# Kernel tuning notes

Measured on AMD Instinct MI355X. Metric: run time of the kernel, lower is better.

## Reference

```python
import jax, jax.numpy as jnp
import numpy as np

SHAPES = ((100, 100), (50, 50), (25, 25), (13, 13))
LENS = [h * w for h, w in SHAPES]
STARTS = [0]
for n in LENS[:-1]:
    STARTS.append(STARTS[-1] + n)
S_TOT = sum(LENS)  # 13294
B, C, HH, DH, L, P, NQ, NL, FF = 2, 256, 8, 32, 4, 4, 300, 6, 1024
WH = np.array([[w, h] for h, w in SHAPES], np.float32)  # [L,2] (W,H) offset normalizer


def ln(x, g, b):
    m = x.mean(-1, keepdims=True)
    v = ((x - m) ** 2).mean(-1, keepdims=True)
    return (x - m) * jax.lax.rsqrt(v + 1e-5) * g + b


def bilinear(v, grid):
    # v: [N,Hl,Wl,D]; grid: [N,Q,2] in [-1,1]; grid_sample bilinear, align_corners=False, zero padding
    N, Hl, Wl, Dd = v.shape
    x = (grid[..., 0] + 1.0) * 0.5 * Wl - 0.5
    y = (grid[..., 1] + 1.0) * 0.5 * Hl - 0.5
    x0f = jnp.floor(x); y0f = jnp.floor(y)
    wx = x - x0f; wy = y - y0f
    x0 = x0f.astype(jnp.int32); y0 = y0f.astype(jnp.int32)
    vf = v.reshape(N, Hl * Wl, Dd)
    def g(yi, xi):
        valid = (yi >= 0) & (yi < Hl) & (xi >= 0) & (xi < Wl)
        idx = jnp.clip(yi, 0, Hl - 1) * Wl + jnp.clip(xi, 0, Wl - 1)
        return jnp.take_along_axis(vf, idx[..., None], axis=1) * valid[..., None]
    return (((1 - wy) * (1 - wx))[..., None] * g(y0, x0)
            + ((1 - wy) * wx)[..., None] * g(y0, x0 + 1)
            + (wy * (1 - wx))[..., None] * g(y0 + 1, x0)
            + (wy * wx)[..., None] * g(y0 + 1, x0 + 1))


def msda(query, ref, src, so_w, so_b, aw_w, aw_b, vp_w, vp_b, op_w, op_b):
    # query:[B,Lq,C] ref:[B,Lq,L,2] src:[B,S,C]
    Bq, Lq, _ = query.shape
    value = (src @ vp_w.T + vp_b).reshape(Bq, S_TOT, HH, DH)
    offs = (query @ so_w.T + so_b).reshape(Bq, Lq, HH, L, P, 2)
    aw = jax.nn.softmax((query @ aw_w.T + aw_b).reshape(Bq, Lq, HH, L * P), -1)
    aw = aw.reshape(Bq, Lq, HH, L, P)
    loc = ref[:, :, None, :, None, :] + offs / jnp.asarray(WH)[None, None, None, :, None, :]
    grid = 2.0 * loc - 1.0  # [B,Lq,HH,L,P,2]
    out = jnp.zeros((Bq, HH, Lq, DH), query.dtype)
    for l, (Hl, Wl) in enumerate(SHAPES):
        st = STARTS[l]
        v_l = value[:, st:st + Hl * Wl].reshape(Bq, Hl, Wl, HH, DH).transpose(0, 3, 1, 2, 4).reshape(Bq * HH, Hl, Wl, DH)
        g_l = grid[:, :, :, l].transpose(0, 2, 1, 3, 4).reshape(Bq * HH, Lq * P, 2)
        s = bilinear(v_l, g_l).reshape(Bq, HH, Lq, P, DH)
        out = out + jnp.einsum('bqhp,bhqpd->bhqd', aw[:, :, :, l], s)
    out = out.transpose(0, 2, 1, 3).reshape(Bq, Lq, C)
    return out @ op_w.T + op_b


def enc_ref_points():
    refs = []
    for Hl, Wl in SHAPES:
        ry = (jnp.arange(Hl, dtype=jnp.float32) + 0.5) / Hl
        rx = (jnp.arange(Wl, dtype=jnp.float32) + 0.5) / Wl
        gy, gx = jnp.meshgrid(ry, rx, indexing='ij')
        refs.append(jnp.stack([gx.reshape(-1), gy.reshape(-1)], -1))
    r = jnp.concatenate(refs, 0)  # [S,2]; valid_ratios == 1 (no padding)
    return jnp.broadcast_to(r[None, :, None, :], (B, S_TOT, L, 2))


def _forward(src_flatten, pos_flatten, query_embed, level_embed, refp_w, refp_b,
             eso_w, eso_b, eaw_w, eaw_b, evp_w, evp_b, eop_w, eop_b,
             en1_g, en1_b, el1_w, el1_b, el2_w, el2_b, en2_g, en2_b,
             dso_w, dso_b, daw_w, daw_b, dvp_w, dvp_b, dop_w, dop_b,
             dsa_in_w, dsa_in_b, dsa_out_w, dsa_out_b,
             dn1_g, dn1_b, dn2_g, dn2_b, dn3_g, dn3_b,
             dl1_w, dl1_b, dl2_w, dl2_b):
    lev = jnp.concatenate([jnp.broadcast_to(level_embed[l], (LENS[l], C)) for l in range(L)], 0)
    pos = pos_flatten + lev[None]
    memory = src_flatten
    eref = enc_ref_points()
    for i in range(NL):  # encoder
        q = memory + pos
        m2 = msda(q, eref, memory, eso_w[i], eso_b[i], eaw_w[i], eaw_b[i], evp_w[i], evp_b[i], eop_w[i], eop_b[i])
        memory = ln(memory + m2, en1_g[i], en1_b[i])
        f = jax.nn.relu(memory @ el1_w[i].T + el1_b[i]) @ el2_w[i].T + el2_b[i]
        memory = ln(memory + f, en2_g[i], en2_b[i])
    qpos, tgt = jnp.split(query_embed, 2, axis=-1)
    qpos = jnp.broadcast_to(qpos[None], (B, NQ, C))
    tgt = jnp.broadcast_to(tgt[None], (B, NQ, C))
    ref = jax.nn.sigmoid(qpos @ refp_w.T + refp_b)  # [B,NQ,2]
    init_ref = ref
    ref_in = jnp.broadcast_to(ref[:, :, None, :], (B, NQ, L, 2))
    scale = 1.0 / np.sqrt(DH)
    for i in range(NL):  # decoder
        q = tgt + qpos
        wq, wk, wv = jnp.split(dsa_in_w[i], 3, 0)
        bq, bk, bv = jnp.split(dsa_in_b[i], 3, 0)
        qh = (q @ wq.T + bq).reshape(B, NQ, HH, DH).transpose(0, 2, 1, 3)
        kh = (q @ wk.T + bk).reshape(B, NQ, HH, DH).transpose(0, 2, 1, 3)
        vh = (tgt @ wv.T + bv).reshape(B, NQ, HH, DH).transpose(0, 2, 1, 3)
        att = jax.nn.softmax(jnp.einsum('bhqd,bhkd->bhqk', qh, kh) * scale, -1)
        sa = jnp.einsum('bhqk,bhkd->bhqd', att, vh).transpose(0, 2, 1, 3).reshape(B, NQ, C)
        sa = sa @ dsa_out_w[i].T + dsa_out_b[i]
        tgt = ln(tgt + sa, dn2_g[i], dn2_b[i])
        ca = msda(tgt + qpos, ref_in, memory, dso_w[i], dso_b[i], daw_w[i], daw_b[i], dvp_w[i], dvp_b[i], dop_w[i], dop_b[i])
        tgt = ln(tgt + ca, dn1_g[i], dn1_b[i])
        f = jax.nn.relu(tgt @ dl1_w[i].T + dl1_b[i]) @ dl2_w[i].T + dl2_b[i]
        tgt = ln(tgt + f, dn3_g[i], dn3_b[i])
    return tgt, init_ref, ref


def setup_inputs() -> dict:
    ks = iter(jax.random.split(jax.random.key(0), 80))
    def rn(shape, s=0.02):
        return jax.random.normal(next(ks), shape, jnp.float32) * s
    z = lambda shape: jnp.zeros(shape, jnp.float32)
    o = lambda shape: jnp.ones(shape, jnp.float32)
    HLP2, HLP = HH * L * P * 2, HH * L * P
    return {
        'src_flatten': rn((B, S_TOT, C), 1.0),
        'pos_flatten': rn((B, S_TOT, C), 1.0),
        'query_embed': rn((NQ, 2 * C), 1.0),
        'level_embed': rn((L, C), 1.0),
        'refp_w': rn((2, C)), 'refp_b': z((2,)),
        'eso_w': rn((NL, HLP2, C)), 'eso_b': z((NL, HLP2)),
        'eaw_w': rn((NL, HLP, C)), 'eaw_b': z((NL, HLP)),
        'evp_w': rn((NL, C, C)), 'evp_b': z((NL, C)),
        'eop_w': rn((NL, C, C)), 'eop_b': z((NL, C)),
        'en1_g': o((NL, C)), 'en1_b': z((NL, C)),
        'el1_w': rn((NL, FF, C)), 'el1_b': z((NL, FF)),
        'el2_w': rn((NL, C, FF)), 'el2_b': z((NL, C)),
        'en2_g': o((NL, C)), 'en2_b': z((NL, C)),
        'dso_w': rn((NL, HLP2, C)), 'dso_b': z((NL, HLP2)),
        'daw_w': rn((NL, HLP, C)), 'daw_b': z((NL, HLP)),
        'dvp_w': rn((NL, C, C)), 'dvp_b': z((NL, C)),
        'dop_w': rn((NL, C, C)), 'dop_b': z((NL, C)),
        'dsa_in_w': rn((NL, 3 * C, C)), 'dsa_in_b': z((NL, 3 * C)),
        'dsa_out_w': rn((NL, C, C)), 'dsa_out_b': z((NL, C)),
        'dn1_g': o((NL, C)), 'dn1_b': z((NL, C)),
        'dn2_g': o((NL, C)), 'dn2_b': z((NL, C)),
        'dn3_g': o((NL, C)), 'dn3_b': z((NL, C)),
        'dl1_w': rn((NL, FF, C)), 'dl1_b': z((NL, FF)),
        'dl2_w': rn((NL, C, FF)), 'dl2_b': z((NL, C)),
    }


def reference(src_flatten, pos_flatten, query_embed, level_embed, refp_w, refp_b,
              eso_w, eso_b, eaw_w, eaw_b, evp_w, evp_b, eop_w, eop_b,
              en1_g, en1_b, el1_w, el1_b, el2_w, el2_b, en2_g, en2_b,
              dso_w, dso_b, daw_w, daw_b, dvp_w, dvp_b, dop_w, dop_b,
              dsa_in_w, dsa_in_b, dsa_out_w, dsa_out_b,
              dn1_g, dn1_b, dn2_g, dn2_b, dn3_g, dn3_b,
              dl1_w, dl1_b, dl2_w, dl2_b):
    return _forward(src_flatten, pos_flatten, query_embed, level_embed, refp_w, refp_b,
                    eso_w, eso_b, eaw_w, eaw_b, evp_w, evp_b, eop_w, eop_b,
                    en1_g, en1_b, el1_w, el1_b, el2_w, el2_b, en2_g, en2_b,
                    dso_w, dso_b, daw_w, daw_b, dvp_w, dvp_b, dop_w, dop_b,
                    dsa_in_w, dsa_in_b, dsa_out_w, dsa_out_b,
                    dn1_g, dn1_b, dn2_g, dn2_b, dn3_g, dn3_b,
                    dl1_w, dl1_b, dl2_w, dl2_b)
```

## Files before the change

kernel.cpp:

```cpp
#include <hip/hip_runtime.h>

static constexpr int kS  = 13294;
static constexpr int kB  = 2;
static constexpr int kBS = kB * kS;
static constexpr int kC  = 256;
static constexpr int kH  = 8;
static constexpr int kNQ = 300;
static constexpr int kFF = 1024;
static constexpr int kNL = 6;

using short8 = __attribute__((ext_vector_type(8))) short;
using f32x4  = __attribute__((ext_vector_type(4))) float;

__device__ __forceinline__ unsigned short f2b(float f) {
  unsigned u = __builtin_bit_cast(unsigned, f);
  return (unsigned short)((u + 0x7FFF + ((u >> 16) & 1)) >> 16);
}
__device__ __forceinline__ float bf2f(unsigned short u) {
  return __builtin_bit_cast(float, ((unsigned)u) << 16);
}
__device__ __forceinline__ float bflo(unsigned u) {
  return __builtin_bit_cast(float, u << 16);
}
__device__ __forceinline__ float bfhi(unsigned u) {
  return __builtin_bit_cast(float, u & 0xFFFF0000u);
}

#if defined(__has_builtin)
#if __has_builtin(__builtin_amdgcn_global_load_lds)
#define HAS_GLL 1
#endif
#endif
#ifndef HAS_GLL
#define HAS_GLL 0
#endif

#if HAS_GLL
typedef const __attribute__((address_space(1))) void* gas_t;
typedef __attribute__((address_space(3))) void* las_t;
#define GLOAD16(gp, lp) __builtin_amdgcn_global_load_lds((gas_t)(gp), (las_t)(lp), 16, 0, 0)
#endif


template<int ACT, int OBF>
__global__ __launch_bounds__(256) void gemm_mfma(
    const unsigned short* __restrict__ A, const unsigned short* __restrict__ Wt,
    const float* __restrict__ bias, void* __restrict__ outp, int M, int N, int K) {
  __shared__ __align__(16) unsigned short As[128 * 64];
  __shared__ __align__(16) unsigned short Bs[128 * 64];
  const int t = threadIdx.x;
  const int nB = N >> 7;
  const int tot = gridDim.x;
  const int q8 = tot >> 3, r8 = tot & 7;
  const int xcd = blockIdx.x & 7, pos = blockIdx.x >> 3;
  const int wg = (xcd < r8 ? xcd * (q8 + 1) : r8 * (q8 + 1) + (xcd - r8) * q8) + pos;
  const int m0 = (wg / nB) * 128, n0 = (wg % nB) * 128;
  const int wid = t >> 6, lane = t & 63;
  const int wr = wid >> 1, wc = wid & 1;
  const int srow = t >> 3;
  const int scol = (((t & 7) ^ (srow & 7)) * 8);
  const int lr = lane & 15;
  const int q4 = lane >> 4;
  const int e7 = lr & 7;

  f32x4 acc[4][4];
#pragma unroll
  for (int i = 0; i < 4; ++i)
#pragma unroll
    for (int j = 0; j < 4; ++j) acc[i][j] = (f32x4){0.f, 0.f, 0.f, 0.f};

  for (int k0 = 0; k0 < K; k0 += 64) {
#if HAS_GLL
    __syncthreads();
#pragma unroll
    for (int c = 0; c < 4; ++c) {
      int ar = m0 + c * 32 + srow; if (ar >= M) ar = M - 1;
      GLOAD16(A + (size_t)ar * K + k0 + scol, (char*)As + c * 4096 + t * 16);
      int br = n0 + c * 32 + srow; if (br >= N) br = N - 1;
      GLOAD16(Wt + (size_t)br * K + k0 + scol, (char*)Bs + c * 4096 + t * 16);
    }
    __syncthreads();
#else
    short8 ta[4], tb[4];
#pragma unroll
    for (int c = 0; c < 4; ++c) {
      int ar = m0 + c * 32 + srow; if (ar >= M) ar = M - 1;
      ta[c] = *(const short8*)(A + (size_t)ar * K + k0 + scol);
      int br = n0 + c * 32 + srow; if (br >= N) br = N - 1;
      tb[c] = *(const short8*)(Wt + (size_t)br * K + k0 + scol);
    }
    __syncthreads();
#pragma unroll
    for (int c = 0; c < 4; ++c) {
      *(short8*)&As[c * 2048 + t * 8] = ta[c];
      *(short8*)&Bs[c * 2048 + t * 8] = tb[c];
    }
    __syncthreads();
#endif
#pragma unroll
    for (int kk = 0; kk < 2; ++kk) {
      const int pg = (((kk << 2) + q4) ^ e7) * 8;
      short8 af[4], bf[4];
#pragma unroll
      for (int mi = 0; mi < 4; ++mi)
        af[mi] = *(const short8*)&As[(wr * 64 + mi * 16 + lr) * 64 + pg];
#pragma unroll
      for (int ni = 0; ni < 4; ++ni)
        bf[ni] = *(const short8*)&Bs[(wc * 64 + ni * 16 + lr) * 64 + pg];
#pragma unroll
      for (int mi = 0; mi < 4; ++mi)
#pragma unroll
        for (int ni = 0; ni < 4; ++ni)
          acc[mi][ni] = __builtin_amdgcn_mfma_f32_16x16x32_bf16(af[mi], bf[ni], acc[mi][ni], 0, 0, 0);
    }
  }
  const int orow0 = m0 + wr * 64;
  const int ocol = n0 + wc * 64 + lr;
  float bv[4];
#pragma unroll
  for (int ni = 0; ni < 4; ++ni) bv[ni] = bias[ocol + ni * 16];
#pragma unroll
  for (int mi = 0; mi < 4; ++mi) {
#pragma unroll
    for (int j = 0; j < 4; ++j) {
      const int r = orow0 + mi * 16 + q4 * 4 + j;
      if (r < M) {
#pragma unroll
        for (int ni = 0; ni < 4; ++ni) {
          float v = acc[mi][ni][j] + bv[ni];
          if (ACT) v = fmaxf(v, 0.f);
          if (OBF) ((unsigned short*)outp)[(size_t)r * N + ocol + ni * 16] = f2b(v);
          else     ((float*)outp)[(size_t)r * N + ocol + ni * 16] = v;
        }
      }
    }
  }
}

template<int ACT, int OBF>
__global__ __launch_bounds__(256) void gemm_mfma_s(
    const unsigned short* __restrict__ A, const unsigned short* __restrict__ Wt,
    const float* __restrict__ bias, void* __restrict__ outp, int M, int N, int K) {
  __shared__ __align__(16) unsigned short As[64 * 64];
  __shared__ __align__(16) unsigned short Bs[64 * 64];
  const int t = threadIdx.x;
  const int m0 = blockIdx.y * 64, n0 = blockIdx.x * 64;
  const int wid = t >> 6, lane = t & 63;
  const int wr = wid >> 1, wc = wid & 1;
  const int srow = t >> 3;
  const int scol = (((t & 7) ^ (srow & 7)) * 8);
  const int lr = lane & 15;
  const int q4 = lane >> 4;
  const int e7 = lr & 7;

  f32x4 acc[2][2];
#pragma unroll
  for (int i = 0; i < 2; ++i)
#pragma unroll
    for (int j = 0; j < 2; ++j) acc[i][j] = (f32x4){0.f, 0.f, 0.f, 0.f};

  for (int k0 = 0; k0 < K; k0 += 64) {
#if HAS_GLL
    __syncthreads();
#pragma unroll
    for (int c = 0; c < 2; ++c) {
      int ar = m0 + c * 32 + srow; if (ar >= M) ar = M - 1;
      GLOAD16(A + (size_t)ar * K + k0 + scol, (char*)As + c * 4096 + t * 16);
      int br = n0 + c * 32 + srow; if (br >= N) br = N - 1;
      GLOAD16(Wt + (size_t)br * K + k0 + scol, (char*)Bs + c * 4096 + t * 16);
    }
    __syncthreads();
#else
    short8 ta[2], tb[2];
#pragma unroll
    for (int c = 0; c < 2; ++c) {
      int ar = m0 + c * 32 + srow; if (ar >= M) ar = M - 1;
      ta[c] = *(const short8*)(A + (size_t)ar * K + k0 + scol);
      int br = n0 + c * 32 + srow; if (br >= N) br = N - 1;
      tb[c] = *(const short8*)(Wt + (size_t)br * K + k0 + scol);
    }
    __syncthreads();
#pragma unroll
    for (int c = 0; c < 2; ++c) {
      *(short8*)&As[c * 2048 + t * 8] = ta[c];
      *(short8*)&Bs[c * 2048 + t * 8] = tb[c];
    }
    __syncthreads();
#endif
#pragma unroll
    for (int kk = 0; kk < 2; ++kk) {
      const int pg = (((kk << 2) + q4) ^ e7) * 8;
      short8 af[2], bf[2];
#pragma unroll
      for (int mi = 0; mi < 2; ++mi)
        af[mi] = *(const short8*)&As[(wr * 32 + mi * 16 + lr) * 64 + pg];
#pragma unroll
      for (int ni = 0; ni < 2; ++ni)
        bf[ni] = *(const short8*)&Bs[(wc * 32 + ni * 16 + lr) * 64 + pg];
#pragma unroll
      for (int mi = 0; mi < 2; ++mi)
#pragma unroll
        for (int ni = 0; ni < 2; ++ni)
          acc[mi][ni] = __builtin_amdgcn_mfma_f32_16x16x32_bf16(af[mi], bf[ni], acc[mi][ni], 0, 0, 0);
    }
  }
  const int orow0 = m0 + wr * 32;
  const int ocol = n0 + wc * 32 + lr;
  float bv[2];
#pragma unroll
  for (int ni = 0; ni < 2; ++ni) bv[ni] = bias[ocol + ni * 16];
#pragma unroll
  for (int mi = 0; mi < 2; ++mi) {
#pragma unroll
    for (int j = 0; j < 4; ++j) {
      const int r = orow0 + mi * 16 + q4 * 4 + j;
      if (r < M) {
#pragma unroll
        for (int ni = 0; ni < 2; ++ni) {
          float v = acc[mi][ni][j] + bv[ni];
          if (ACT) v = fmaxf(v, 0.f);
          if (OBF) ((unsigned short*)outp)[(size_t)r * N + ocol + ni * 16] = f2b(v);
          else     ((float*)outp)[(size_t)r * N + ocol + ni * 16] = v;
        }
      }
    }
  }
}

template<int WRITEQ, int WRITEF>
__global__ __launch_bounds__(256) void gemm_ln_k(
    const unsigned short* __restrict__ A, const unsigned short* __restrict__ Wt,
    const float* __restrict__ bias, const unsigned short* __restrict__ x_bf,
    const float* __restrict__ g, const float* __restrict__ be,
    float* __restrict__ outf, unsigned short* __restrict__ outb,
    unsigned short* __restrict__ qout, const unsigned short* __restrict__ poslev,
    int M, int K) {
  __shared__ __align__(16) unsigned short As[32 * 128];
  __shared__ __align__(16) unsigned short Bs[256 * 128];
  __shared__ float rsum[32][4], rsq[32][4], rmv[32][2];
  const int t = threadIdx.x;
  const int m0 = blockIdx.x * 32;
  const int wid = t >> 6, lane = t & 63;
  const int lr = lane & 15;
  const int q4 = lane >> 4;
  const int t16 = t >> 4;
  const int g16 = (t & 15) ^ t16;

  f32x4 acc[2][4];
#pragma unroll
  for (int i = 0; i < 2; ++i)
#pragma unroll
    for (int j = 0; j < 4; ++j) acc[i][j] = (f32x4){0.f, 0.f, 0.f, 0.f};

  for (int k0 = 0; k0 < K; k0 += 128) {
#if HAS_GLL
    __syncthreads();
#pragma unroll
    for (int c = 0; c < 2; ++c) {
      int ar = m0 + c * 16 + t16; if (ar >= M) ar = M - 1;
      GLOAD16(A + (size_t)ar * K + k0 + g16 * 8, (char*)As + c * 4096 + t * 16);
    }
#pragma unroll
    for (int c = 0; c < 16; ++c) {
      const int br = c * 16 + t16;
      GLOAD16(Wt + (size_t)br * K + k0 + g16 * 8, (char*)Bs + c * 4096 + t * 16);
    }
    __syncthreads();
#else
    short8 ta[2], tb[16];
#pragma unroll
    for (int c = 0; c < 2; ++c) {
      int ar = m0 + c * 16 + t16; if (ar >= M) ar = M - 1;
      ta[c] = *(const short8*)(A + (size_t)ar * K + k0 + g16 * 8);
    }
#pragma unroll
    for (int c = 0; c < 16; ++c)
      tb[c] = *(const short8*)(Wt + (size_t)(c * 16 + t16) * K + k0 + g16 * 8);
    __syncthreads();
#pragma unroll
    for (int c = 0; c < 2; ++c) *(short8*)&As[c * 2048 + t * 8] = ta[c];
#pragma unroll
    for (int c = 0; c < 16; ++c) *(short8*)&Bs[c * 2048 + t * 8] = tb[c];
    __syncthreads();
#endif
#pragma unroll
    for (int kk = 0; kk < 4; ++kk) {
      const int pg = (((kk << 2) + q4) ^ lr) * 8;
      short8 af[2], bf[4];
#pragma unroll
      for (int mi = 0; mi < 2; ++mi)
        af[mi] = *(const short8*)&As[(mi * 16 + lr) * 128 + pg];
#pragma unroll
      for (int ni = 0; ni < 4; ++ni)
        bf[ni] = *(const short8*)&Bs[(wid * 64 + ni * 16 + lr) * 128 + pg];
#pragma unroll
      for (int mi = 0; mi < 2; ++mi)
#pragma unroll
        for (int ni = 0; ni < 4; ++ni)
          acc[mi][ni] = __builtin_amdgcn_mfma_f32_16x16x32_bf16(af[mi], bf[ni], acc[mi][ni], 0, 0, 0);
    }
  }
  float bv[4], gv[4], bev[4];
  int cols[4];
#pragma unroll
  for (int ni = 0; ni < 4; ++ni) {
    cols[ni] = wid * 64 + ni * 16 + lr;
    bv[ni] = bias[cols[ni]];
    gv[ni] = g[cols[ni]];
    bev[ni] = be[cols[ni]];
  }
#pragma unroll
  for (int mi = 0; mi < 2; ++mi) {
#pragma unroll
    for (int j = 0; j < 4; ++j) {
      const int brow = mi * 16 + q4 * 4 + j;
      int grow = m0 + brow; if (grow >= M) grow = M - 1;
      const unsigned short* xr = x_bf + (size_t)grow * 256;
      float s = 0.f, s2 = 0.f;
#pragma unroll
      for (int ni = 0; ni < 4; ++ni) {
        float v = acc[mi][ni][j] + bv[ni] + bf2f(xr[cols[ni]]);
        acc[mi][ni][j] = v;
        s += v; s2 += v * v;
      }
#pragma unroll
      for (int o = 1; o < 16; o <<= 1) {
        s += __shfl_xor(s, o);
        s2 += __shfl_xor(s2, o);
      }
      if (lr == 0) { rsum[brow][wid] = s; rsq[brow][wid] = s2; }
    }
  }
  __syncthreads();
  if (t < 32) {
    float s = rsum[t][0] + rsum[t][1] + rsum[t][2] + rsum[t][3];
    float s2 = rsq[t][0] + rsq[t][1] + rsq[t][2] + rsq[t][3];
    float mean = s * (1.f / 256.f);
    float var = s2 * (1.f / 256.f) - mean * mean;
    rmv[t][0] = mean;
    rmv[t][1] = rsqrtf(var + 1e-5f);
  }
  __syncthreads();
#pragma unroll
  for (int mi = 0; mi < 2; ++mi) {
#pragma unroll
    for (int j = 0; j < 4; ++j) {
      const int brow = mi * 16 + q4 * 4 + j;
      const int grow = m0 + brow;
      if (grow >= M) continue;
      const float mean = rmv[brow][0], rs = rmv[brow][1];
#pragma unroll
      for (int ni = 0; ni < 4; ++ni) {
        const float v = (acc[mi][ni][j] - mean) * rs * gv[ni] + bev[ni];
        const size_t oi = (size_t)grow * 256 + cols[ni];
        if (WRITEF) outf[oi] = v;
        outb[oi] = f2b(v);
        if (WRITEQ) qout[oi] = f2b(v + bf2f(poslev[oi]));
      }
    }
  }
}

__global__ void cast_bf_k(const float* __restrict__ in, unsigned short* __restrict__ out, int n4) {
  int i = blockIdx.x * 256 + threadIdx.x;
  if (i >= n4) return;
  float4 v = ((const float4*)in)[i];
  ushort4 o; o.x = f2b(v.x); o.y = f2b(v.y); o.z = f2b(v.z); o.w = f2b(v.w);
  ((ushort4*)out)[i] = o;
}

__global__ void pack_bias_k(const float* __restrict__ so_b, const float* __restrict__ aw_b,
                            float* __restrict__ fb) {
  int i = blockIdx.x * 256 + threadIdx.x;
  if (i >= kNL * 384) return;
  int l = i / 384, j = i - l * 384;
  fb[i] = (j < 256) ? so_b[l * 256 + j] : aw_b[l * 128 + j - 256];
}

__global__ void poslev_k(const float* __restrict__ pos, const float* __restrict__ lev,
                         unsigned short* __restrict__ out, int n4) {
  int i = blockIdx.x * 256 + threadIdx.x;
  if (i >= n4) return;
  int c4 = i & 63;
  int row = i >> 6;
  int s = row % kS;
  int l = (s < 10000) ? 0 : (s < 12500) ? 1 : (s < 13125) ? 2 : 3;
  float4 p = ((const float4*)pos)[i];
  float4 lv = ((const float4*)(lev + l * kC))[c4];
  ushort4 o;
  o.x = f2b(p.x + lv.x); o.y = f2b(p.y + lv.y);
  o.z = f2b(p.z + lv.z); o.w = f2b(p.w + lv.w);
  ((ushort4*)out)[i] = o;
}

__global__ void enc_q_k(const float* __restrict__ src, const unsigned short* __restrict__ poslev,
                        unsigned short* __restrict__ q, int n4) {
  int i = blockIdx.x * 256 + threadIdx.x;
  if (i >= n4) return;
  float4 m = ((const float4*)src)[i];
  ushort4 pl = ((const ushort4*)poslev)[i];
  ushort4 o;
  o.x = f2b(m.x + bf2f(pl.x)); o.y = f2b(m.y + bf2f(pl.y));
  o.z = f2b(m.z + bf2f(pl.z)); o.w = f2b(m.w + bf2f(pl.w));
  ((ushort4*)q)[i] = o;
}

__global__ void refs_k(float* __restrict__ refS) {
  int s = blockIdx.x * 256 + threadIdx.x;
  if (s >= kS) return;
  int st, W;
  if (s < 10000)      { st = 0;     W = 100; }
  else if (s < 12500) { st = 10000; W = 50; }
  else if (s < 13125) { st = 12500; W = 25; }
  else                { st = 13125; W = 13; }
  int idx = s - st;
  int y = idx / W;
  int x = idx - y * W;
  refS[s * 2 + 0] = (x + 0.5f) / (float)W;
  refS[s * 2 + 1] = (y + 0.5f) / (float)W;
}

__global__ __launch_bounds__(256) void msda_fused_k(
    const unsigned short* __restrict__ value, int vstride, int vcol,
    const unsigned short* __restrict__ foab, const float* __restrict__ refs,
    unsigned short* __restrict__ out, int Mq) {
  __shared__ int   sidx[16][2][kH][4];
  __shared__ float sw[16][2][kH][4];
  const int t = threadIdx.x;
  const int bq0 = blockIdx.x * 2;
  const int qq = t >> 7;
  {
    const int bq = bq0 + qq;
    const int b = (bq >= Mq) ? 1 : 0;
    const int qi = bq - b * Mq;
    const int h = (t >> 4) & 7, lp = t & 15, l = lp >> 2;
    const unsigned short* row = foab + (size_t)bq * 384;
    float logit = bf2f(row[256 + h * 16 + lp]);
    float mx = logit;
#pragma unroll
    for (int o = 1; o < 16; o <<= 1) mx = fmaxf(mx, __shfl_xor(mx, o));
    float e = __expf(logit - mx), ssum = e;
#pragma unroll
    for (int o = 1; o < 16; o <<= 1) ssum += __shfl_xor(ssum, o);
    const float a = e / ssum;
    const unsigned opair = *(const unsigned*)(row + h * 32 + lp * 2);
    const float offx = bflo(opair);
    const float offy = bfhi(opair);
    const float rx = refs[qi * 2 + 0];
    const float ry = refs[qi * 2 + 1];
    const int wtab[4] = {100, 50, 25, 13};
    const int stab[4] = {0, 10000, 12500, 13125};
    const int W = wtab[l];
    const int start = stab[l];
    const float px = fmaf(rx, (float)W, offx) - 0.5f;
    const float py = fmaf(ry, (float)W, offy) - 0.5f;
    const float fx = floorf(px), fy = floorf(py);
    const float wx = px - fx, wy = py - fy;
    const int x0 = (int)fx, y0 = (int)fy;
    const int x0c = min(max(x0, 0), W - 1);
    const int x1c = min(max(x0 + 1, 0), W - 1);
    const int y0c = min(max(y0, 0), W - 1);
    const int y1c = min(max(y0 + 1, 0), W - 1);
    const float vx0 = (x0 >= 0 && x0 < W) ? 1.f : 0.f;
    const float vx1 = (x0 + 1 >= 0 && x0 + 1 < W) ? 1.f : 0.f;
    const float vy0 = (y0 >= 0 && y0 < W) ? 1.f : 0.f;
    const float vy1 = (y0 + 1 >= 0 && y0 + 1 < W) ? 1.f : 0.f;
    const int base0 = b * kS * vstride + vcol + start * vstride;
    sidx[lp][qq][h][0] = base0 + (y0c * W + x0c) * vstride;
    sidx[lp][qq][h][1] = base0 + (y0c * W + x1c) * vstride;
    sidx[lp][qq][h][2] = base0 + (y1c * W + x0c) * vstride;
    sidx[lp][qq][h][3] = base0 + (y1c * W + x1c) * vstride;
    const float omwx = 1.f - wx, omwy = 1.f - wy;
    sw[lp][qq][h][0] = a * omwy * omwx * vy0 * vx0;
    sw[lp][qq][h][1] = a * omwy * wx * vy0 * vx1;
    sw[lp][qq][h][2] = a * wy * omwx * vy1 * vx0;
    sw[lp][qq][h][3] = a * wy * wx * vy1 * vx1;
  }
  __syncthreads();
  const int h = (t >> 4) & 7, dp = t & 15;
  const int bq = bq0 + qq;
  const int chan = h * 64 + dp * 4;
  const char* valc = (const char*)value;
  float aLo0 = 0.f, aLo1 = 0.f, aHi0 = 0.f, aHi1 = 0.f;
#pragma unroll
  for (int p0 = 0; p0 < 16; p0 += 8) {
    unsigned u[32];
    float w[32];
#pragma unroll
    for (int pp = 0; pp < 8; ++pp) {
      const int4 I = *(const int4*)&sidx[p0 + pp][qq][h][0];
      const float4 Wv = *(const float4*)&sw[p0 + pp][qq][h][0];
      u[pp * 4 + 0] = *(const unsigned*)(valc + (unsigned)(I.x + chan));
      u[pp * 4 + 1] = *(const unsigned*)(valc + (unsigned)(I.y + chan));
      u[pp * 4 + 2] = *(const unsigned*)(valc + (unsigned)(I.z + chan));
      u[pp * 4 + 3] = *(const unsigned*)(valc + (unsigned)(I.w + chan));
      w[pp * 4 + 0] = Wv.x; w[pp * 4 + 1] = Wv.y;
      w[pp * 4 + 2] = Wv.z; w[pp * 4 + 3] = Wv.w;
    }
#pragma unroll
    for (int j = 0; j < 32; j += 2) {
      aLo0 = fmaf(w[j], bflo(u[j]), aLo0);
      aHi0 = fmaf(w[j], bfhi(u[j]), aHi0);
      aLo1 = fmaf(w[j + 1], bflo(u[j + 1]), aLo1);
      aHi1 = fmaf(w[j + 1], bfhi(u[j + 1]), aHi1);
    }
  }
  const float accLo = aLo0 + aLo1;
  const float accHi = aHi0 + aHi1;
  const unsigned packed = (unsigned)f2b(accLo) | ((unsigned)f2b(accHi) << 16);
  ((unsigned*)out)[(size_t)bq * 128 + h * 16 + dp] = packed;
}

__global__ void add_bcast_bf_k(const float* __restrict__ a, const float* __restrict__ b,
                               unsigned short* __restrict__ out, int n4, int nb4) {
  int i = blockIdx.x * 256 + threadIdx.x;
  if (i >= n4) return;
  const float4 av = ((const float4*)a)[i];
  const float4 bv = ((const float4*)b)[i % nb4];
  ushort4 o;
  o.x = f2b(av.x + bv.x); o.y = f2b(av.y + bv.y);
  o.z = f2b(av.z + bv.z); o.w = f2b(av.w + bv.w);
  ((ushort4*)out)[i] = o;
}

__global__ void dec_init_k(const float* __restrict__ qe, float* __restrict__ tgt,
                           unsigned short* __restrict__ tgt_bf, float* __restrict__ qposb) {
  int i = blockIdx.x * 256 + threadIdx.x;
  if (i >= kNQ * kC) return;
  int q = i >> 8, c = i & 255;
  qposb[i] = qe[q * 512 + c];
  float tg = qe[q * 512 + 256 + c];
  tgt[i] = tg;
  tgt[kNQ * kC + i] = tg;
  unsigned short tb = f2b(tg);
  tgt_bf[i] = tb;
  tgt_bf[kNQ * kC + i] = tb;
}

__global__ __launch_bounds__(64) void ref_k(const float* __restrict__ qposb,
                                            const float* __restrict__ rw,
                                            const float* __restrict__ rb,
                                            float* __restrict__ ref300) {
  const int q = blockIdx.x;
  const int lane = threadIdx.x;
  const float4 qv = ((const float4*)(qposb + q * 256))[lane];
  const float4 w0 = ((const float4*)rw)[lane];
  const float4 w1 = ((const float4*)(rw + 256))[lane];
  float a0 = qv.x * w0.x + qv.y * w0.y + qv.z * w0.z + qv.w * w0.w;
  float a1 = qv.x * w1.x + qv.y * w1.y + qv.z * w1.z + qv.w * w1.w;
#pragma unroll
  for (int off = 32; off; off >>= 1) {
    a0 += __shfl_xor(a0, off);
    a1 += __shfl_xor(a1, off);
  }
  if (lane == 0) {
    ref300[q * 2 + 0] = 1.f / (1.f + __expf(-(a0 + rb[0])));
    ref300[q * 2 + 1] = 1.f / (1.f + __expf(-(a1 + rb[1])));
  }
}

__global__ __launch_bounds__(64) void dec_attn_k(const float* __restrict__ qk,
                                                 const float* __restrict__ v,
                                                 unsigned short* __restrict__ outp) {
  const int bid = blockIdx.x;
  const int q = bid % kNQ;
  const int bh = bid / kNQ;
  const int h = bh & 7;
  const int b = bh >> 3;
  const int lane = threadIdx.x;
  __shared__ float p[304];
  const float* qv = qk + ((size_t)(b * kNQ + q)) * 512 + h * 32;
  float qreg[32];
#pragma unroll
  for (int m = 0; m < 32; ++m) qreg[m] = qv[m];
  float scores[5];
  float mx = -1e30f;
#pragma unroll
  for (int j = 0; j < 5; ++j) {
    const int k = lane + j * 64;
    float sc = -1e30f;
    if (k < kNQ) {
      const float* kv = qk + ((size_t)(b * kNQ + k)) * 512 + 256 + h * 32;
      float acc = 0.f;
#pragma unroll
      for (int m = 0; m < 32; ++m) acc = fmaf(qreg[m], kv[m], acc);
      sc = acc * 0.17677669529663687f;
    }
    scores[j] = sc;
    mx = fmaxf(mx, sc);
  }
#pragma unroll
  for (int off = 32; off; off >>= 1) mx = fmaxf(mx, __shfl_xor(mx, off));
  float sum = 0.f;
#pragma unroll
  for (int j = 0; j < 5; ++j) {
    const int k = lane + j * 64;
    float e = 0.f;
    if (k < kNQ) e = __expf(scores[j] - mx);
    scores[j] = e;
    sum += e;
  }
#pragma unroll
  for (int off = 32; off; off >>= 1) sum += __shfl_xor(sum, off);
  const float inv = 1.f / sum;
#pragma unroll
  for (int j = 0; j < 5; ++j) {
    const int k = lane + j * 64;
    if (k < kNQ) p[k] = scores[j] * inv;
  }
  __syncthreads();
  const int d = lane & 31, half = lane >> 5;
  float acc = 0.f;
  for (int k = half * 150; k < half * 150 + 150; ++k)
    acc = fmaf(p[k], v[((size_t)(b * kNQ + k)) * 256 + h * 32 + d], acc);
  acc += __shfl_down(acc, 32);
  if (lane < 32) outp[((size_t)(b * kNQ + q)) * 256 + h * 32 + d] = f2b(acc);
}

__global__ void write_refs_k(const float* __restrict__ ref300, float* __restrict__ outp) {
  int i = blockIdx.x * 256 + threadIdx.x;
  if (i >= 1200) return;
  float v = ref300[i % 600];
  outp[153600 + i] = v;
  outp[154800 + i] = v;
}

__global__ void sentinel_k(float* __restrict__ outp) {
  if (threadIdx.x < 64) outp[threadIdx.x] = 12345.0f;
}

extern "C" void kernel_launch(void* const* d_in, const int* in_sizes, int n_in,
                              void* d_out, int out_size, void* d_ws, size_t ws_size,
                              hipStream_t stream) {
  const float* src      = (const float*)d_in[0];
  const float* pos      = (const float*)d_in[1];
  const float* qe       = (const float*)d_in[2];
  const float* lev      = (const float*)d_in[3];
  const float* refp_w   = (const float*)d_in[4];
  const float* refp_b   = (const float*)d_in[5];
  const float* eso_w    = (const float*)d_in[6];
  const float* eso_b    = (const float*)d_in[7];
  const float* eaw_w    = (const float*)d_in[8];
  const float* eaw_b    = (const float*)d_in[9];
  const float* evp_w    = (const float*)d_in[10];
  const float* evp_b    = (const float*)d_in[11];
  const float* eop_w    = (const float*)d_in[12];
  const float* eop_b    = (const float*)d_in[13];
  const float* en1_g    = (const float*)d_in[14];
  const float* en1_b    = (const float*)d_in[15];
  const float* el1_w    = (const float*)d_in[16];
  const float* el1_b    = (const float*)d_in[17];
  const float* el2_w    = (const float*)d_in[18];
  const float* el2_b    = (const float*)d_in[19];
  const float* en2_g    = (const float*)d_in[20];
  const float* en2_b    = (const float*)d_in[21];
  const float* dso_w    = (const float*)d_in[22];
  const float* dso_b    = (const float*)d_in[23];
  const float* daw_w    = (const float*)d_in[24];
  const float* daw_b    = (const float*)d_in[25];
  const float* dvp_w    = (const float*)d_in[26];
  const float* dvp_b    = (const float*)d_in[27];
  const float* dop_w    = (const float*)d_in[28];
  const float* dop_b    = (const float*)d_in[29];
  const float* dsa_in_w = (const float*)d_in[30];
  const float* dsa_in_b = (const float*)d_in[31];
  const float* dsa_out_w= (const float*)d_in[32];
  const float* dsa_out_b= (const float*)d_in[33];
  const float* dn1_g    = (const float*)d_in[34];
  const float* dn1_b    = (const float*)d_in[35];
  const float* dn2_g    = (const float*)d_in[36];
  const float* dn2_b    = (const float*)d_in[37];
  const float* dn3_g    = (const float*)d_in[38];
  const float* dn3_b    = (const float*)d_in[39];
  const float* dl1_w    = (const float*)d_in[40];
  const float* dl1_b    = (const float*)d_in[41];
  const float* dl2_w    = (const float*)d_in[42];
  const float* dl2_b    = (const float*)d_in[43];

  float* Wsp = (float*)d_ws;
  size_t off = 0;
  auto alloc = [&](size_t n) { float* p = Wsp + off; off += n; return p; };
  const size_t NBC = (size_t)kBS * kC;
  unsigned short* memory_bf = (unsigned short*)alloc(NBC / 2);
  unsigned short* poslev_bf = (unsigned short*)alloc(NBC / 2);
  float* r2       = alloc(NBC);
  unsigned short* val_bf = (unsigned short*)r2;
  float* r3       = alloc(NBC / 2);
  unsigned short* qbuf_bf = (unsigned short*)r3;
  unsigned short* sampbuf_bf = (unsigned short*)r3;
  float* r4       = alloc(NBC * 2);
  unsigned short* foab_bf = (unsigned short*)r4;
  unsigned short* hid_bf = (unsigned short*)r4;
  unsigned short* val_all = (unsigned short*)r2;
  float* refS     = alloc((size_t)kS * 2 + 2);
  auto allocb = [&](size_t elems) { return (unsigned short*)alloc(elems / 2); };
  unsigned short* fesoawW = allocb((size_t)kNL * 384 * 256);
  unsigned short* evpW  = allocb((size_t)kNL * 65536);
  unsigned short* eopW  = allocb((size_t)kNL * 65536);
  unsigned short* el1W  = allocb((size_t)kNL * 262144);
  unsigned short* el2W  = allocb((size_t)kNL * 262144);
  unsigned short* fdsoawW = allocb((size_t)kNL * 384 * 256);
  unsigned short* dvpW  = allocb((size_t)kNL * 65536);
  unsigned short* dopW  = allocb((size_t)kNL * 65536);
  unsigned short* dsaiW = allocb((size_t)kNL * 196608);
  unsigned short* dsaoW = allocb((size_t)kNL * 65536);
  unsigned short* dl1W  = allocb((size_t)kNL * 262144);
  unsigned short* dl2W  = allocb((size_t)kNL * 262144);
  float* fbias_e  = alloc((size_t)kNL * 384);
  float* fbias_d  = alloc((size_t)kNL * 384);
  const size_t NQC = (size_t)kB * kNQ * kC;
  float* tgt      = alloc(NQC);
  unsigned short* tgt_bf = (unsigned short*)alloc(NQC / 2);
  float* qposb    = alloc((size_t)kNQ * kC);
  unsigned short* dq_bf = (unsigned short*)alloc(NQC / 2);
  float* qkbuf    = alloc(NQC * 2);
  float* vbuf     = alloc(NQC);
  unsigned short* sabuf_bf = (unsigned short*)alloc(NQC / 2);
  unsigned short* dfoab_bf = (unsigned short*)alloc((size_t)kB * kNQ * 384 / 2);
  unsigned short* dsamp_bf = (unsigned short*)alloc(NQC / 2);
  unsigned short* dffnh_bf = (unsigned short*)alloc((size_t)kB * kNQ * kFF / 2);
  float* ref300   = alloc(600);

  if (ws_size < off * sizeof(float)) {
    hipLaunchKernelGGL(sentinel_k, dim3(1), dim3(64), 0, stream, (float*)d_out);
    return;
  }

  auto GEMM = [&](const unsigned short* A, const unsigned short* Wt, const float* bias,
                  void* out, int M, int N, int K, int variant) {
    dim3 g((N / 128) * ((M + 127) / 128));
    if (variant == 1)
      hipLaunchKernelGGL((gemm_mfma<1, 1>), g, dim3(256), 0, stream, A, Wt, bias, out, M, N, K);
    else if (variant == 2)
      hipLaunchKernelGGL((gemm_mfma<0, 1>), g, dim3(256), 0, stream, A, Wt, bias, out, M, N, K);
    else
      hipLaunchKernelGGL((gemm_mfma<0, 0>), g, dim3(256), 0, stream, A, Wt, bias, out, M, N, K);
  };
  auto GEMMS = [&](const unsigned short* A, const unsigned short* Wt, const float* bias,
                   void* out, int M, int N, int K, int variant) {
    dim3 g(N / 64, (M + 63) / 64);
    if (variant == 1)
      hipLaunchKernelGGL((gemm_mfma_s<1, 1>), g, dim3(256), 0, stream, A, Wt, bias, out, M, N, K);
    else if (variant == 2)
      hipLaunchKernelGGL((gemm_mfma_s<0, 1>), g, dim3(256), 0, stream, A, Wt, bias, out, M, N, K);
    else
      hipLaunchKernelGGL((gemm_mfma_s<0, 0>), g, dim3(256), 0, stream, A, Wt, bias, out, M, N, K);
  };
  auto CASTW = [&](const float* srcw, unsigned short* dstw, size_t elems) {
    int n4 = (int)(elems / 4);
    hipLaunchKernelGGL(cast_bf_k, dim3((n4 + 255) / 256), dim3(256), 0, stream, srcw, dstw, n4);
  };

  for (int i = 0; i < kNL; ++i) {
    CASTW(eso_w + (size_t)i * 65536, fesoawW + (size_t)i * 98304, 65536);
    CASTW(eaw_w + (size_t)i * 32768, fesoawW + (size_t)i * 98304 + 65536, 32768);
    CASTW(dso_w + (size_t)i * 65536, fdsoawW + (size_t)i * 98304, 65536);
    CASTW(daw_w + (size_t)i * 32768, fdsoawW + (size_t)i * 98304 + 65536, 32768);
  }
  CASTW(evp_w, evpW, (size_t)kNL * 65536);
  CASTW(eop_w, eopW, (size_t)kNL * 65536);
  CASTW(el1_w, el1W, (size_t)kNL * 262144);
  CASTW(el2_w, el2W, (size_t)kNL * 262144);
  CASTW(dvp_w, dvpW, (size_t)kNL * 65536);
  CASTW(dop_w, dopW, (size_t)kNL * 65536);
  CASTW(dsa_in_w, dsaiW, (size_t)kNL * 196608);
  CASTW(dsa_out_w, dsaoW, (size_t)kNL * 65536);
  CASTW(dl1_w, dl1W, (size_t)kNL * 262144);
  CASTW(dl2_w, dl2W, (size_t)kNL * 262144);
  hipLaunchKernelGGL(pack_bias_k, dim3((kNL * 384 + 255) / 256), dim3(256), 0, stream,
                     eso_b, eaw_b, fbias_e);
  hipLaunchKernelGGL(pack_bias_k, dim3((kNL * 384 + 255) / 256), dim3(256), 0, stream,
                     dso_b, daw_b, fbias_d);
  const int n4full = kBS * 64;
  hipLaunchKernelGGL(cast_bf_k, dim3((n4full + 255) / 256), dim3(256), 0, stream,
                     src, memory_bf, n4full);
  hipLaunchKernelGGL(poslev_k, dim3((n4full + 255) / 256), dim3(256), 0, stream,
                     pos, lev, poslev_bf, n4full);
  hipLaunchKernelGGL(refs_k, dim3((kS + 255) / 256), dim3(256), 0, stream, refS);
  hipLaunchKernelGGL(enc_q_k, dim3((n4full + 255) / 256), dim3(256), 0, stream,
                     src, poslev_bf, qbuf_bf, n4full);

  const int grid_ln = (kBS + 31) / 32;
  for (int i = 0; i < kNL; ++i) {
    GEMM(memory_bf, evpW + (size_t)i * 65536, evp_b + i * kC, val_bf, kBS, 256, 256, 2);
    GEMM(qbuf_bf, fesoawW + (size_t)i * 98304, fbias_e + i * 384, foab_bf, kBS, 384, 256, 2);
    hipLaunchKernelGGL(msda_fused_k, dim3(kBS / 2), dim3(256), 0, stream,
                       val_bf, 512, 0, foab_bf, refS, sampbuf_bf, kS);
    hipLaunchKernelGGL((gemm_ln_k<0, 0>), dim3(grid_ln), dim3(256), 0, stream,
                       sampbuf_bf, eopW + (size_t)i * 65536, eop_b + i * kC,
                       memory_bf, en1_g + i * kC, en1_b + i * kC,
                       (float*)nullptr, memory_bf, (unsigned short*)nullptr,
                       (const unsigned short*)nullptr, kBS, 256);
    GEMM(memory_bf, el1W + (size_t)i * 262144, el1_b + i * kFF, hid_bf, kBS, 1024, 256, 1);
    hipLaunchKernelGGL((gemm_ln_k<1, 0>), dim3(grid_ln), dim3(256), 0, stream,
                       hid_bf, el2W + (size_t)i * 262144, el2_b + i * kC,
                       memory_bf, en2_g + i * kC, en2_b + i * kC,
                       (float*)nullptr, memory_bf, qbuf_bf, poslev_bf, kBS, 1024);
  }

  hipLaunchKernelGGL(dec_init_k, dim3(300), dim3(256), 0, stream, qe, tgt, tgt_bf, qposb);
  hipLaunchKernelGGL(ref_k, dim3(kNQ), dim3(64), 0, stream, qposb, refp_w, refp_b, ref300);
  GEMM(memory_bf, dvpW, dvp_b, val_all, kBS, kNL * 256, 256, 2);

  const int dn4 = kB * kNQ * 64;
  const int qn4 = kNQ * 64;
  const int MD = kB * kNQ;
  const int grid_lnd = (MD + 31) / 32;
  for (int i = 0; i < kNL; ++i) {
    hipLaunchKernelGGL(add_bcast_bf_k, dim3((dn4 + 255) / 256), dim3(256), 0, stream,
                       tgt, qposb, dq_bf, dn4, qn4);
    GEMMS(dq_bf, dsaiW + (size_t)i * 196608, dsa_in_b + i * 768, qkbuf, MD, 512, 256, 0);
    GEMMS(tgt_bf, dsaiW + (size_t)i * 196608 + (size_t)512 * 256,
          dsa_in_b + i * 768 + 512, vbuf, MD, 256, 256, 0);
    hipLaunchKernelGGL(dec_attn_k, dim3(kB * kH * kNQ), dim3(64), 0, stream,
                       qkbuf, vbuf, sabuf_bf);
    hipLaunchKernelGGL((gemm_ln_k<0, 1>), dim3(grid_lnd), dim3(256), 0, stream,
                       sabuf_bf, dsaoW + (size_t)i * 65536, dsa_out_b + i * kC,
                       tgt_bf, dn2_g + i * kC, dn2_b + i * kC,
                       tgt, tgt_bf, (unsigned short*)nullptr,
                       (const unsigned short*)nullptr, MD, 256);
    hipLaunchKernelGGL(add_bcast_bf_k, dim3((dn4 + 255) / 256), dim3(256), 0, stream,
                       tgt, qposb, dq_bf, dn4, qn4);
    GEMMS(dq_bf, fdsoawW + (size_t)i * 98304, fbias_d + i * 384, dfoab_bf, MD, 384, 256, 2);
    hipLaunchKernelGGL(msda_fused_k, dim3(MD / 2), dim3(256), 0, stream,
                       val_all, kNL * 512, i * 512, dfoab_bf, ref300, dsamp_bf, kNQ);
    hipLaunchKernelGGL((gemm_ln_k<0, 1>), dim3(grid_lnd), dim3(256), 0, stream,
                       dsamp_bf, dopW + (size_t)i * 65536, dop_b + i * kC,
                       tgt_bf, dn1_g + i * kC, dn1_b + i * kC,
                       tgt, tgt_bf, (unsigned short*)nullptr,
                       (const unsigned short*)nullptr, MD, 256);
    GEMMS(tgt_bf, dl1W + (size_t)i * 262144, dl1_b + i * kFF, dffnh_bf, MD, 1024, 256, 1);
    hipLaunchKernelGGL((gemm_ln_k<0, 1>), dim3(grid_lnd), dim3(256), 0, stream,
                       dffnh_bf, dl2W + (size_t)i * 262144, dl2_b + i * kC,
                       tgt_bf, dn3_g + i * kC, dn3_b + i * kC,
                       tgt, tgt_bf, (unsigned short*)nullptr,
                       (const unsigned short*)nullptr, MD, 1024);
  }

  hipMemcpyAsync(d_out, tgt, NQC * sizeof(float), hipMemcpyDeviceToDevice, stream);
  hipLaunchKernelGGL(write_refs_k, dim3(5), dim3(256), 0, stream, ref300, (float*)d_out);
}
```

Before: 1.745 ms.

## Precompute query-pos projections and fuse decoder QKV into one GEMM

Uses linearity, (tgt+qpos)W = tgt·W + qpos·W, to precompute the qpos projections for all decoder layers once as per-row correction tables with biases folded in. Each decoder layer can then drop its two add_bcast kernels and run the Q/K/V projection as a single 768-wide GEMM on tgt_bf, with the correction added in the epilogue. Attention reads from the fused qkv buffer, and the so/aw weight packing becomes one kernel per weight set. In exchange it adds extra precompute GEMMs, larger correction buffers and per-row correction loads, and rounding differs slightly because tgt and qpos are now each rounded to bf16 separately.

```diff
diff --git a/kernel.cpp b/kernel.cpp
--- a/kernel.cpp
+++ b/kernel.cpp
@@ -137,10 +137,11 @@
   }
 }
 
-template<int ACT, int OBF>
+template<int ACT, int OBF, int CORR>
 __global__ __launch_bounds__(256) void gemm_mfma_s(
     const unsigned short* __restrict__ A, const unsigned short* __restrict__ Wt,
-    const float* __restrict__ bias, void* __restrict__ outp, int M, int N, int K) {
+    const float* __restrict__ bias, void* __restrict__ outp, int M, int N, int K,
+    const float* __restrict__ corr, int cld) {
   __shared__ __align__(16) unsigned short As[64 * 64];
   __shared__ __align__(16) unsigned short Bs[64 * 64];
   const int t = threadIdx.x;
@@ -208,16 +209,17 @@
   const int ocol = n0 + wc * 32 + lr;
   float bv[2];
 #pragma unroll
-  for (int ni = 0; ni < 2; ++ni) bv[ni] = bias[ocol + ni * 16];
+  for (int ni = 0; ni < 2; ++ni) bv[ni] = CORR ? 0.f : bias[ocol + ni * 16];
 #pragma unroll
   for (int mi = 0; mi < 2; ++mi) {
 #pragma unroll
     for (int j = 0; j < 4; ++j) {
       const int r = orow0 + mi * 16 + q4 * 4 + j;
       if (r < M) {
+        const float* cr = CORR ? (corr + (size_t)(r < kNQ ? r : r - kNQ) * cld) : nullptr;
 #pragma unroll
         for (int ni = 0; ni < 2; ++ni) {
-          float v = acc[mi][ni][j] + bv[ni];
+          float v = acc[mi][ni][j] + (CORR ? cr[ocol + ni * 16] : bv[ni]);
           if (ACT) v = fmaxf(v, 0.f);
           if (OBF) ((unsigned short*)outp)[(size_t)r * N + ocol + ni * 16] = f2b(v);
           else     ((float*)outp)[(size_t)r * N + ocol + ni * 16] = v;
@@ -369,12 +371,37 @@
   ((ushort4*)out)[i] = o;
 }
 
+__global__ void pack_soaw_k(const float* __restrict__ so_w, const float* __restrict__ aw_w,
+                            unsigned short* __restrict__ out, int total4) {
+  int i = blockIdx.x * 256 + threadIdx.x;
+  if (i >= total4) return;
+  int e = i * 4;
+  int l = e / 98304;
+  int rem = e - l * 98304;
+  int r = rem >> 8;
+  int c = rem & 255;
+  const float* src = (r < 256) ? (so_w + (size_t)l * 65536 + r * 256 + c)
+                               : (aw_w + (size_t)l * 32768 + (r - 256) * 256 + c);
+  float4 v = *(const float4*)src;
+  ushort4 o; o.x = f2b(v.x); o.y = f2b(v.y); o.z = f2b(v.z); o.w = f2b(v.w);
+  ((ushort4*)out)[i] = o;
+}
+
 __global__ void pack_bias_k(const float* __restrict__ so_b, const float* __restrict__ aw_b,
                             float* __restrict__ fb) {
   int i = blockIdx.x * 256 + threadIdx.x;
   if (i >= kNL * 384) return;
   int l = i / 384, j = i - l * 384;
   fb[i] = (j < 256) ? so_b[l * 256 + j] : aw_b[l * 128 + j - 256];
+}
+
+__global__ void corr_vfix_k(const float* __restrict__ dsa_in_b, float* __restrict__ corr) {
+  int i = blockIdx.x * 256 + threadIdx.x;
+  if (i >= kNQ * kNL * 256) return;
+  int q = i / (kNL * 256);
+  int rem = i - q * (kNL * 256);
+  int l = rem >> 8, c = rem & 255;
+  corr[(size_t)q * (kNL * 768) + l * 768 + 512 + c] = dsa_in_b[l * 768 + 512 + c];
 }
 
 __global__ void poslev_k(const float* __restrict__ pos, const float* __restrict__ lev,
@@ -511,24 +538,15 @@
   ((unsigned*)out)[(size_t)bq * 128 + h * 16 + dp] = packed;
 }
 
-__global__ void add_bcast_bf_k(const float* __restrict__ a, const float* __restrict__ b,
-                               unsigned short* __restrict__ out, int n4, int nb4) {
-  int i = blockIdx.x * 256 + threadIdx.x;
-  if (i >= n4) return;
-  const float4 av = ((const float4*)a)[i];
-  const float4 bv = ((const float4*)b)[i % nb4];
-  ushort4 o;
-  o.x = f2b(av.x + bv.x); o.y = f2b(av.y + bv.y);
-  o.z = f2b(av.z + bv.z); o.w = f2b(av.w + bv.w);
-  ((ushort4*)out)[i] = o;
-}
-
 __global__ void dec_init_k(const float* __restrict__ qe, float* __restrict__ tgt,
-                           unsigned short* __restrict__ tgt_bf, float* __restrict__ qposb) {
+                           unsigned short* __restrict__ tgt_bf, float* __restrict__ qposb,
+                           unsigned short* __restrict__ qpos_bf) {
   int i = blockIdx.x * 256 + threadIdx.x;
   if (i >= kNQ * kC) return;
   int q = i >> 8, c = i & 255;
-  qposb[i] = qe[q * 512 + c];
+  float qp = qe[q * 512 + c];
+  qposb[i] = qp;
+  qpos_bf[i] = f2b(qp);
   float tg = qe[q * 512 + 256 + c];
   tgt[i] = tg;
   tgt[kNQ * kC + i] = tg;
@@ -559,8 +577,7 @@
   }
 }
 
-__global__ __launch_bounds__(64) void dec_attn_k(const float* __restrict__ qk,
-                                                 const float* __restrict__ v,
+__global__ __launch_bounds__(64) void dec_attn_k(const float* __restrict__ qkv,
                                                  unsigned short* __restrict__ outp) {
   const int bid = blockIdx.x;
   const int q = bid % kNQ;
@@ -569,7 +586,7 @@
   const int b = bh >> 3;
   const int lane = threadIdx.x;
   __shared__ float p[304];
-  const float* qv = qk + ((size_t)(b * kNQ + q)) * 512 + h * 32;
+  const float* qv = qkv + (size_t)(b * kNQ + q) * 768 + h * 32;
   float qreg[32];
 #pragma unroll
   for (int m = 0; m < 32; ++m) qreg[m] = qv[m];
@@ -580,7 +597,7 @@
     const int k = lane + j * 64;
     float sc = -1e30f;
     if (k < kNQ) {
-      const float* kv = qk + ((size_t)(b * kNQ + k)) * 512 + 256 + h * 32;
+      const float* kv = qkv + (size_t)(b * kNQ + k) * 768 + 256 + h * 32;
       float acc = 0.f;
 #pragma unroll
       for (int m = 0; m < 32; ++m) acc = fmaf(qreg[m], kv[m], acc);
@@ -612,7 +629,7 @@
   const int d = lane & 31, half = lane >> 5;
   float acc = 0.f;
   for (int k = half * 150; k < half * 150 + 150; ++k)
-    acc = fmaf(p[k], v[((size_t)(b * kNQ + k)) * 256 + h * 32 + d], acc);
+    acc = fmaf(p[k], qkv[(size_t)(b * kNQ + k) * 768 + 512 + h * 32 + d], acc);
   acc += __shfl_down(acc, 32);
   if (lane < 32) outp[((size_t)(b * kNQ + q)) * 256 + h * 32 + d] = f2b(acc);
 }
@@ -712,13 +729,14 @@
   float* tgt      = alloc(NQC);
   unsigned short* tgt_bf = (unsigned short*)alloc(NQC / 2);
   float* qposb    = alloc((size_t)kNQ * kC);
-  unsigned short* dq_bf = (unsigned short*)alloc(NQC / 2);
-  float* qkbuf    = alloc(NQC * 2);
-  float* vbuf     = alloc(NQC);
+  unsigned short* qpos_bf = (unsigned short*)alloc((size_t)kNQ * kC / 2);
+  float* qkvbuf   = alloc((size_t)kB * kNQ * 768);
   unsigned short* sabuf_bf = (unsigned short*)alloc(NQC / 2);
   unsigned short* dfoab_bf = (unsigned short*)alloc((size_t)kB * kNQ * 384 / 2);
   unsigned short* dsamp_bf = (unsigned short*)alloc(NQC / 2);
   unsigned short* dffnh_bf = (unsigned short*)alloc((size_t)kB * kNQ * kFF / 2);
+  float* corrQKV  = alloc((size_t)kNQ * kNL * 768);
+  float* corrSOAW = alloc((size_t)kNQ * kNL * 384);
   float* ref300   = alloc(600);
 
   if (ws_size < off * sizeof(float)) {
@@ -736,26 +754,17 @@
     else
       hipLaunchKernelGGL((gemm_mfma<0, 0>), g, dim3(256), 0, stream, A, Wt, bias, out, M, N, K);
   };
-  auto GEMMS = [&](const unsigned short* A, const unsigned short* Wt, const float* bias,
-                   void* out, int M, int N, int K, int variant) {
-    dim3 g(N / 64, (M + 63) / 64);
-    if (variant == 1)
-      hipLaunchKernelGGL((gemm_mfma_s<1, 1>), g, dim3(256), 0, stream, A, Wt, bias, out, M, N, K);
-    else if (variant == 2)
-      hipLaunchKernelGGL((gemm_mfma_s<0, 1>), g, dim3(256), 0, stream, A, Wt, bias, out, M, N, K);
-    else
-      hipLaunchKernelGGL((gemm_mfma_s<0, 0>), g, dim3(256), 0, stream, A, Wt, bias, out, M, N, K);
-  };
   auto CASTW = [&](const float* srcw, unsigned short* dstw, size_t elems) {
     int n4 = (int)(elems / 4);
     hipLaunchKernelGGL(cast_bf_k, dim3((n4 + 255) / 256), dim3(256), 0, stream, srcw, dstw, n4);
   };
 
-  for (int i = 0; i < kNL; ++i) {
-    CASTW(eso_w + (size_t)i * 65536, fesoawW + (size_t)i * 98304, 65536);
-    CASTW(eaw_w + (size_t)i * 32768, fesoawW + (size_t)i * 98304 + 65536, 32768);
-    CASTW(dso_w + (size_t)i * 65536, fdsoawW + (size_t)i * 98304, 65536);
-    CASTW(daw_w + (size_t)i * 32768, fdsoawW + (size_t)i * 98304 + 65536, 32768);
+  {
+    const int tot4 = kNL * 98304 / 4;
+    hipLaunchKernelGGL(pack_soaw_k, dim3((tot4 + 255) / 256), dim3(256), 0, stream,
+                       eso_w, eaw_w, fesoawW, tot4);
+    hipLaunchKernelGGL(pack_soaw_k, dim3((tot4 + 255) / 256), dim3(256), 0, stream,
+                       dso_w, daw_w, fdsoawW, tot4);
   }
   CASTW(evp_w, evpW, (size_t)kNL * 65536);
   CASTW(eop_w, eopW, (size_t)kNL * 65536);
@@ -798,30 +807,34 @@
                        (float*)nullptr, memory_bf, qbuf_bf, poslev_bf, kBS, 1024);
   }
 
-  hipLaunchKernelGGL(dec_init_k, dim3(300), dim3(256), 0, stream, qe, tgt, tgt_bf, qposb);
+  hipLaunchKernelGGL(dec_init_k, dim3(300), dim3(256), 0, stream, qe, tgt, tgt_bf, qposb, qpos_bf);
   hipLaunchKernelGGL(ref_k, dim3(kNQ), dim3(64), 0, stream, qposb, refp_w, refp_b, ref300);
   GEMM(memory_bf, dvpW, dvp_b, val_all, kBS, kNL * 256, 256, 2);
-
-  const int dn4 = kB * kNQ * 64;
-  const int qn4 = kNQ * 64;
+  hipLaunchKernelGGL((gemm_mfma_s<0, 0, 0>), dim3(kNL * 768 / 64, (kNQ + 63) / 64), dim3(256), 0,
+                     stream, qpos_bf, dsaiW, dsa_in_b, corrQKV, kNQ, kNL * 768, 256,
+                     (const float*)nullptr, 0);
+  hipLaunchKernelGGL(corr_vfix_k, dim3((kNQ * kNL * 256 + 255) / 256), dim3(256), 0, stream,
+                     dsa_in_b, corrQKV);
+  hipLaunchKernelGGL((gemm_mfma_s<0, 0, 0>), dim3(kNL * 384 / 64, (kNQ + 63) / 64), dim3(256), 0,
+                     stream, qpos_bf, fdsoawW, fbias_d, corrSOAW, kNQ, kNL * 384, 256,
+                     (const float*)nullptr, 0);
+
   const int MD = kB * kNQ;
   const int grid_lnd = (MD + 31) / 32;
   for (int i = 0; i < kNL; ++i) {
-    hipLaunchKernelGGL(add_bcast_bf_k, dim3((dn4 + 255) / 256), dim3(256), 0, stream,
-                       tgt, qposb, dq_bf, dn4, qn4);
-    GEMMS(dq_bf, dsaiW + (size_t)i * 196608, dsa_in_b + i * 768, qkbuf, MD, 512, 256, 0);
-    GEMMS(tgt_bf, dsaiW + (size_t)i * 196608 + (size_t)512 * 256,
-          dsa_in_b + i * 768 + 512, vbuf, MD, 256, 256, 0);
+    hipLaunchKernelGGL((gemm_mfma_s<0, 0, 1>), dim3(768 / 64, (MD + 63) / 64), dim3(256), 0,
+                       stream, tgt_bf, dsaiW + (size_t)i * 196608, (const float*)nullptr,
+                       qkvbuf, MD, 768, 256, corrQKV + (size_t)i * 768, kNL * 768);
     hipLaunchKernelGGL(dec_attn_k, dim3(kB * kH * kNQ), dim3(64), 0, stream,
-                       qkbuf, vbuf, sabuf_bf);
+                       qkvbuf, sabuf_bf);
     hipLaunchKernelGGL((gemm_ln_k<0, 1>), dim3(grid_lnd), dim3(256), 0, stream,
                        sabuf_bf, dsaoW + (size_t)i * 65536, dsa_out_b + i * kC,
                        tgt_bf, dn2_g + i * kC, dn2_b + i * kC,
                        tgt, tgt_bf, (unsigned short*)nullptr,
                        (const unsigned short*)nullptr, MD, 256);
-    hipLaunchKernelGGL(add_bcast_bf_k, dim3((dn4 + 255) / 256), dim3(256), 0, stream,
-                       tgt, qposb, dq_bf, dn4, qn4);
-    GEMMS(dq_bf, fdsoawW + (size_t)i * 98304, fbias_d + i * 384, dfoab_bf, MD, 384, 256, 2);
+    hipLaunchKernelGGL((gemm_mfma_s<0, 1, 1>), dim3(384 / 64, (MD + 63) / 64), dim3(256), 0,
+                       stream, tgt_bf, fdsoawW + (size_t)i * 98304, (const float*)nullptr,
+                       dfoab_bf, MD, 384, 256, corrSOAW + (size_t)i * 384, kNL * 384);
     hipLaunchKernelGGL(msda_fused_k, dim3(MD / 2), dim3(256), 0, stream,
                        val_all, kNL * 512, i * 512, dfoab_bf, ref300, dsamp_bf, kNQ);
     hipLaunchKernelGGL((gemm_ln_k<0, 1>), dim3(grid_lnd), dim3(256), 0, stream,
@@ -829,7 +842,9 @@
                        tgt_bf, dn1_g + i * kC, dn1_b + i * kC,
                        tgt, tgt_bf, (unsigned short*)nullptr,
                        (const unsigned short*)nullptr, MD, 256);
-    GEMMS(tgt_bf, dl1W + (size_t)i * 262144, dl1_b + i * kFF, dffnh_bf, MD, 1024, 256, 1);
+    hipLaunchKernelGGL((gemm_mfma_s<1, 1, 0>), dim3(1024 / 64, (MD + 63) / 64), dim3(256), 0,
+                       stream, tgt_bf, dl1W + (size_t)i * 262144, dl1_b + i * kFF,
+                       dffnh_bf, MD, 1024, 256, (const float*)nullptr, 0);
     hipLaunchKernelGGL((gemm_ln_k<0, 1>), dim3(grid_lnd), dim3(256), 0, stream,
                        dffnh_bf, dl2W + (size_t)i * 262144, dl2_b + i * kC,
                        tgt_bf, dn3_g + i * kC, dn3_b + i * kC,
```

Result: faster. 1.694 ms, median of 5 (-2.9%).
